# Optimization experiments

Measured on AMD Instinct MI355X. Metric: run time of the kernel, lower is better.

The kernel has to match this reference:

```python
import jax, jax.numpy as jnp
import numpy as np

D = 2048       # hidden / input / output width
DEPTH = 9      # infinite_depth (layer default)


def _infinite_layer(x, inf_w, cls_w, cls_b):
    """Faithful vectorized InfiniteNeuralLayer.forward.

    Original per-(sample, j, depth) Python loops build a circulant rotation
    matrix M = cos*I + sin*(shift_down - shift_up) and apply it 3x per depth
    with angles inf_w[depth, j, 0..2]. The rotated state never depends on x,
    so we carry one state row per output index j and scan over the 27 angle
    steps, expressing M @ s as cos*s + sin*(roll(s,1) - roll(s,-1)).
    infinite_biases is unused in the original forward and is omitted.
    """
    dim = x.shape[1]
    classical = x @ cls_w + cls_b                      # [B, dim]
    # angles per j per depth step: (DEPTH, dim_j, 3) -> sequence (DEPTH*3, dim_j)
    angles = jnp.transpose(inf_w[:, :, :3], (0, 2, 1)).reshape(-1, dim)
    init = jnp.full((dim, dim), 1.0 / np.sqrt(dim), dtype=x.dtype)  # [j, state]

    def step(s, a):
        c = jnp.cos(a)[:, None]
        sn = jnp.sin(a)[:, None]
        s_new = c * s + sn * (jnp.roll(s, 1, axis=1) - jnp.roll(s, -1, axis=1))
        return s_new, None

    state, _ = jax.lax.scan(step, init, angles)        # [dim_j, dim]
    p = state[:, 0] ** 2                               # |state[0]|^2 per j
    return jnp.tanh(classical + p[None, :])            # broadcast over batch


def setup_inputs() -> dict:
    key = jax.random.key(0)
    ks = jax.random.split(key, 16)
    s = 0.02  # keep activations in sane range (original uses raw randn)
    f = jax.random.normal
    return {
        "x":      f(ks[0], (2048, D), dtype=jnp.float32),
        "w0":     f(ks[1], (D, D), dtype=jnp.float32) * s,
        "b0":     f(ks[2], (D,), dtype=jnp.float32) * s,
        "w1":     f(ks[3], (D, D), dtype=jnp.float32) * s,
        "b1":     f(ks[4], (D,), dtype=jnp.float32) * s,
        "inf_w1": f(ks[5], (DEPTH, D, D), dtype=jnp.float32),
        "cls_w1": f(ks[6], (D, D), dtype=jnp.float32) * s,
        "cls_b1": f(ks[7], (D,), dtype=jnp.float32) * s,
        "w2":     f(ks[8], (D, D), dtype=jnp.float32) * s,
        "b2":     f(ks[9], (D,), dtype=jnp.float32) * s,
        "inf_w2": f(ks[10], (DEPTH, D, D), dtype=jnp.float32),
        "cls_w2": f(ks[11], (D, D), dtype=jnp.float32) * s,
        "cls_b2": f(ks[12], (D,), dtype=jnp.float32) * s,
        "w3":     f(ks[13], (D, D), dtype=jnp.float32) * s,
        "b3":     f(ks[14], (D,), dtype=jnp.float32) * s,
    }


def reference(x, w0, b0, w1, b1, inf_w1, cls_w1, cls_b1,
              w2, b2, inf_w2, cls_w2, cls_b2, w3, b3):
    h = jax.nn.relu(x @ w0 + b0)
    h = jax.nn.relu(h @ w1 + b1)
    h = _infinite_layer(h, inf_w1, cls_w1, cls_b1)
    h = jax.nn.relu(h @ w2 + b2)
    h = _infinite_layer(h, inf_w2, cls_w2, cls_b2)
    return jax.nn.relu(h @ w3 + b3)
```

## Files before the change

kernel.cpp:

```cpp
#include <hip/hip_runtime.h>
#include <hip/hip_bf16.h>


#define DD 2048
#define DEPTH 9

#define BM 128
#define BN 64
#define BK 64
#define NT (DD / BK)
#define ABUF (BM * BK)
#define BBUF (BN * BK)

typedef __attribute__((ext_vector_type(8))) short short8;
typedef __attribute__((ext_vector_type(4))) float f32x4;

__device__ __forceinline__ unsigned short f2bf(float f) {
  unsigned u = __float_as_uint(f);
  u += 0x7FFFu + ((u >> 16) & 1u);
  return (unsigned short)(u >> 16);
}

__global__ __launch_bounds__(256) void prep_kernel(
    const float* __restrict__ w0, const float* __restrict__ w1,
    unsigned short* __restrict__ wts, const float* __restrict__ x,
    unsigned short* __restrict__ xb, const float* __restrict__ infw1,
    const float* __restrict__ infw2, const float* __restrict__ clsb1,
    const float* __restrict__ clsb2, float* __restrict__ padd1,
    float* __restrict__ padd2) {
  int b = blockIdx.x;
  int tid = threadIdx.x;
  if (b < 8192) {
    __shared__ float tile[32][33];
    int z = b >> 12;
    int t = b & 4095;
    const float* src = z ? w1 : w0;
    unsigned short* dst = wts + (size_t)z * DD * DD;
    int bx = (t & 63) * 32;
    int by = (t >> 6) * 32;
    int tx = tid & 31, ty = tid >> 5;
#pragma unroll
    for (int i = ty; i < 32; i += 8)
      tile[i][tx] = src[(size_t)(by + i) * DD + bx + tx];
    __syncthreads();
#pragma unroll
    for (int i = ty; i < 32; i += 8)
      dst[(size_t)(bx + i) * DD + by + tx] = f2bf(tile[tx][i]);
  } else if (b < 12288) {
    int i = (b - 8192) * 256 + tid;
    float4 v = reinterpret_cast<const float4*>(x)[i];
    ushort4 o;
    o.x = f2bf(v.x); o.y = f2bf(v.y); o.z = f2bf(v.z); o.w = f2bf(v.w);
    reinterpret_cast<ushort4*>(xb)[i] = o;
  } else {
    int jj = (b - 12288) * 256 + tid;
    int layer = jj >> 11;
    int j = jj & 2047;
    const float* inf_w = layer ? infw2 : infw1;
    const float* cls_b = layer ? clsb2 : clsb1;
    float* padd = layer ? padd2 : padd1;
    float prod = 1.0f;
#pragma unroll
    for (int d = 0; d < DEPTH; ++d) {
      const float* row = inf_w + ((size_t)d * DD + j) * DD;
      prod *= cosf(row[0]) * cosf(row[1]) * cosf(row[2]);
    }
    padd[j] = cls_b[j] + prod * prod * (1.0f / (float)DD);
  }
}


__device__ __forceinline__ void gload_lds16(const unsigned short* g,
                                            unsigned short* l) {
  __builtin_amdgcn_global_load_lds(
      (const __attribute__((address_space(1))) void*)g,
      (__attribute__((address_space(3))) void*)l, 16, 0, 0);
}

template <int EPI>
__global__ __launch_bounds__(256) void gemm_kernel(
    const unsigned short* __restrict__ A, const unsigned short* __restrict__ Bt,
    const float* __restrict__ bias, unsigned short* __restrict__ Cb,
    float* __restrict__ Cf, const float* __restrict__ tsrc,
    unsigned short* __restrict__ tdst) {
  const int N = DD, K = DD;
  __shared__ __align__(16) unsigned char smem[73728];
  unsigned short* As = (unsigned short*)smem;
  unsigned short* Bs = (unsigned short*)(smem + 3 * ABUF * 2);

  int tid = threadIdx.x;
  int wid = tid >> 6, lane = tid & 63;
  int wr = wid >> 1, wc = wid & 1;
  int lr = lane & 15;
  int lg = lane >> 4;

  int bid = blockIdx.x;
  int swz = (bid & 7) * 64 + (bid >> 3);
  int bcol = (swz & 31) * BN;
  int brow = (swz >> 5) * BM;

  const unsigned short* Abase = A + (size_t)brow * K;
  const unsigned short* Bbase = Bt + (size_t)bcol * K;

  auto stage = [&](int buf, int tile) {
    int kt = tile * BK;
#pragma unroll
    for (int r = 0; r < 4; ++r) {
      int chunk = r * 256 + tid;
      int row = chunk >> 3;
      int sp = chunk & 7;
      int kof = (sp ^ ((row >> 1) & 7)) * 8;
      gload_lds16(Abase + (size_t)row * K + kt + kof,
                  As + buf * ABUF + (size_t)(r * 256 + wid * 64) * 8);
    }
#pragma unroll
    for (int r = 0; r < 2; ++r) {
      int chunk = r * 256 + tid;
      int row = chunk >> 3;
      int sp = chunk & 7;
      int kof = (sp ^ ((row >> 1) & 7)) * 8;
      gload_lds16(Bbase + (size_t)row * K + kt + kof,
                  Bs + buf * BBUF + (size_t)(r * 256 + wid * 64) * 8);
    }
  };

  f32x4 acc[4][2];
#pragma unroll
  for (int i = 0; i < 4; ++i)
#pragma unroll
    for (int j = 0; j < 2; ++j) acc[i][j] = f32x4{0.f, 0.f, 0.f, 0.f};

  auto compute = [&](int buf) {
#pragma unroll
    for (int ks = 0; ks < 2; ++ks) {
      short8 a[4], b[2];
#pragma unroll
      for (int mt = 0; mt < 4; ++mt) {
        int row = wr * 64 + mt * 16 + lr;
        int slot = (ks * 4 + lg) ^ ((row >> 1) & 7);
        a[mt] = *reinterpret_cast<const short8*>(
            &As[buf * ABUF + row * BK + slot * 8]);
      }
#pragma unroll
      for (int nt = 0; nt < 2; ++nt) {
        int row = wc * 32 + nt * 16 + lr;
        int slot = (ks * 4 + lg) ^ ((row >> 1) & 7);
        b[nt] = *reinterpret_cast<const short8*>(
            &Bs[buf * BBUF + row * BK + slot * 8]);
      }
      __builtin_amdgcn_s_setprio(1);
#pragma unroll
      for (int mt = 0; mt < 4; ++mt)
#pragma unroll
        for (int nt = 0; nt < 2; ++nt)
          acc[mt][nt] = __builtin_amdgcn_mfma_f32_16x16x32_bf16(
              a[mt], b[nt], acc[mt][nt], 0, 0, 0);
      __builtin_amdgcn_s_setprio(0);
    }
  };

  auto step = [&](int buf, int pf_tile, int wcase) {
    if (wcase == 0) asm volatile("s_waitcnt vmcnt(12)" ::: "memory");
    else if (wcase == 1) asm volatile("s_waitcnt vmcnt(6)" ::: "memory");
    else asm volatile("s_waitcnt vmcnt(0)" ::: "memory");
    __builtin_amdgcn_s_barrier();
    __builtin_amdgcn_sched_barrier(0);
    compute(buf);
    asm volatile("s_waitcnt lgkmcnt(0)" ::: "memory");
    __builtin_amdgcn_s_barrier();
    __builtin_amdgcn_sched_barrier(0);
    if (pf_tile < NT) stage(pf_tile % 3, pf_tile);
  };

  stage(0, 0); stage(1, 1); stage(2, 2);
#pragma unroll 1
  for (int i = 0; i < 10; ++i) {
    int t = 3 * i;
    step(0, t + 3, 0);
    step(1, t + 4, 0);
    step(2, t + 5, 0);
  }
  step(0, NT, 1);
  step(1, NT, 2);

  {
    float* et = reinterpret_cast<float*>(smem);
    __syncthreads();
#pragma unroll
    for (int nt = 0; nt < 2; ++nt) {
      int colb = wc * 32 + nt * 16 + lr;
      float bs = bias[bcol + colb];
#pragma unroll
      for (int mt = 0; mt < 4; ++mt) {
#pragma unroll
        for (int i = 0; i < 4; ++i) {
          int rowb = wr * 64 + mt * 16 + lg * 4 + i;
          float v = acc[mt][nt][i] + bs;
          v = (EPI == 1) ? tanhf(v) : fmaxf(v, 0.0f);
          et[rowb * 68 + colb] = v;
        }
      }
    }
    __syncthreads();
#pragma unroll
    for (int it = 0; it < 4; ++it) {
      int chunk = it * 256 + tid;
      int rowb = chunk >> 3;
      int c8 = (chunk & 7) * 8;
      float4 v0 = *reinterpret_cast<const float4*>(&et[rowb * 68 + c8]);
      float4 v1 = *reinterpret_cast<const float4*>(&et[rowb * 68 + c8 + 4]);
      size_t g = (size_t)(brow + rowb) * N + bcol + c8;
      if (EPI == 2) {
        *reinterpret_cast<float4*>(&Cf[g]) = v0;
        *reinterpret_cast<float4*>(&Cf[g + 4]) = v1;
      } else {
        uint4 o;
        o.x = (unsigned)f2bf(v0.x) | ((unsigned)f2bf(v0.y) << 16);
        o.y = (unsigned)f2bf(v0.z) | ((unsigned)f2bf(v0.w) << 16);
        o.z = (unsigned)f2bf(v1.x) | ((unsigned)f2bf(v1.y) << 16);
        o.w = (unsigned)f2bf(v1.z) | ((unsigned)f2bf(v1.w) << 16);
        *reinterpret_cast<uint4*>(&Cb[g]) = o;
      }
    }
  }

  if (tsrc != nullptr) {
    float* ft = reinterpret_cast<float*>(smem);
    __syncthreads();
#pragma unroll 1
    for (int t2 = 0; t2 < 2; ++t2) {
      int tau = bid * 2 + t2;
      int bx = (tau & 31) * 64;
      int by = (tau >> 5) * 64;
      if (t2) __syncthreads();
#pragma unroll
      for (int it = 0; it < 4; ++it) {
        int idx = it * 256 + tid;
        int r = idx >> 4, c4 = (idx & 15) * 4;
        float4 v = *reinterpret_cast<const float4*>(
            &tsrc[(size_t)(by + r) * DD + bx + c4]);
        ft[r * 65 + c4 + 0] = v.x;
        ft[r * 65 + c4 + 1] = v.y;
        ft[r * 65 + c4 + 2] = v.z;
        ft[r * 65 + c4 + 3] = v.w;
      }
      __syncthreads();
#pragma unroll
      for (int it = 0; it < 4; ++it) {
        int idx = it * 256 + tid;
        int n = idx >> 4, kq = idx & 15;
        ushort4 o;
        o.x = f2bf(ft[(kq * 4 + 0) * 65 + n]);
        o.y = f2bf(ft[(kq * 4 + 1) * 65 + n]);
        o.z = f2bf(ft[(kq * 4 + 2) * 65 + n]);
        o.w = f2bf(ft[(kq * 4 + 3) * 65 + n]);
        *reinterpret_cast<ushort4*>(&tdst[(size_t)(bx + n) * DD + by + kq * 4]) = o;
      }
    }
  }
}


extern "C" void kernel_launch(void* const* d_in, const int* in_sizes, int n_in,
                              void* d_out, int out_size, void* d_ws,
                              size_t ws_size, hipStream_t stream) {
  const float* x     = (const float*)d_in[0];
  const float* w0    = (const float*)d_in[1];
  const float* b0    = (const float*)d_in[2];
  const float* w1    = (const float*)d_in[3];
  const float* b1    = (const float*)d_in[4];
  const float* infw1 = (const float*)d_in[5];
  const float* clsw1 = (const float*)d_in[6];
  const float* clsb1 = (const float*)d_in[7];
  const float* w2    = (const float*)d_in[8];
  const float* b2    = (const float*)d_in[9];
  const float* infw2 = (const float*)d_in[10];
  const float* clsw2 = (const float*)d_in[11];
  const float* clsb2 = (const float*)d_in[12];
  const float* w3    = (const float*)d_in[13];
  const float* b3    = (const float*)d_in[14];
  float* out = (float*)d_out;

  char* ws = (char*)d_ws;
  const size_t MB = 1ull << 20;
  const size_t DDe = (size_t)DD * DD;
  unsigned short* buf0 = (unsigned short*)ws;
  unsigned short* buf1 = (unsigned short*)(ws + 8 * MB);
  unsigned short* wts  = (unsigned short*)(ws + 16 * MB);
  float* padd1 = (float*)(ws + 64 * MB);
  float* padd2 = padd1 + DD;

  prep_kernel<<<12304, 256, 0, stream>>>(w0, w1, wts, x, buf0, infw1, infw2,
                                         clsb1, clsb2, padd1, padd2);

  dim3 gg((DD / BM) * (DD / BN));
  gemm_kernel<0><<<gg, 256, 0, stream>>>(buf0, wts + 0 * DDe, b0,    buf1,
                                         nullptr, clsw1, wts + 2 * DDe);
  gemm_kernel<0><<<gg, 256, 0, stream>>>(buf1, wts + 1 * DDe, b1,    buf0,
                                         nullptr, w2,    wts + 3 * DDe);
  gemm_kernel<1><<<gg, 256, 0, stream>>>(buf0, wts + 2 * DDe, padd1, buf1,
                                         nullptr, clsw2, wts + 4 * DDe);
  gemm_kernel<0><<<gg, 256, 0, stream>>>(buf1, wts + 3 * DDe, b2,    buf0,
                                         nullptr, w3,    wts + 5 * DDe);
  gemm_kernel<1><<<gg, 256, 0, stream>>>(buf0, wts + 4 * DDe, padd2, buf1,
                                         nullptr, nullptr, nullptr);
  gemm_kernel<2><<<gg, 256, 0, stream>>>(buf1, wts + 5 * DDe, b3,    nullptr,
                                         out, nullptr, nullptr);
}
```

Measured before the change: 184.6 us.

## Enlarge GEMM tile to 128x128 with 8 waves splitting K

Widens the block tile from 128x64 to 128x128 and runs it with 512 threads. The 8 waves are arranged as four 64x64 output quadrants, each split across two waves that handle the two K halves of every 64-wide tile. Partial sums are reduced through LDS in the epilogue before bias and activation are applied. This raises operand reuse per loaded byte and halves the block count. In exchange it adds a cross-wave reduction, uses more LDS and more accumulator registers, and redistributes the transpose side-work over fewer blocks.

```diff
diff --git a/kernel.cpp b/kernel.cpp
--- a/kernel.cpp
+++ b/kernel.cpp
@@ -6,7 +6,7 @@
 #define DEPTH 9
 
 #define BM 128
-#define BN 64
+#define BN 128
 #define BK 64
 #define NT (DD / BK)
 #define ABUF (BM * BK)
@@ -78,26 +78,28 @@
 }
 
 template <int EPI>
-__global__ __launch_bounds__(256) void gemm_kernel(
+__global__ __launch_bounds__(512, 2) void gemm_kernel(
     const unsigned short* __restrict__ A, const unsigned short* __restrict__ Bt,
     const float* __restrict__ bias, unsigned short* __restrict__ Cb,
     float* __restrict__ Cf, const float* __restrict__ tsrc,
     unsigned short* __restrict__ tdst) {
   const int N = DD, K = DD;
-  __shared__ __align__(16) unsigned char smem[73728];
+  __shared__ __align__(16) unsigned char smem[98304];
   unsigned short* As = (unsigned short*)smem;
   unsigned short* Bs = (unsigned short*)(smem + 3 * ABUF * 2);
 
   int tid = threadIdx.x;
   int wid = tid >> 6, lane = tid & 63;
-  int wr = wid >> 1, wc = wid & 1;
+  int pos = wid >> 1;
+  int h = wid & 1;
+  int pr = pos >> 1, pc = pos & 1;
   int lr = lane & 15;
   int lg = lane >> 4;
 
   int bid = blockIdx.x;
-  int swz = (bid & 7) * 64 + (bid >> 3);
-  int bcol = (swz & 31) * BN;
-  int brow = (swz >> 5) * BM;
+  int swz = (bid & 7) * 32 + (bid >> 3);
+  int bcol = (swz & 15) * BN;
+  int brow = (swz >> 4) * BM;
 
   const unsigned short* Abase = A + (size_t)brow * K;
   const unsigned short* Bbase = Bt + (size_t)bcol * K;
@@ -105,63 +107,60 @@
   auto stage = [&](int buf, int tile) {
     int kt = tile * BK;
 #pragma unroll
-    for (int r = 0; r < 4; ++r) {
-      int chunk = r * 256 + tid;
+    for (int r = 0; r < 2; ++r) {
+      int chunk = r * 512 + tid;
       int row = chunk >> 3;
       int sp = chunk & 7;
       int kof = (sp ^ ((row >> 1) & 7)) * 8;
       gload_lds16(Abase + (size_t)row * K + kt + kof,
-                  As + buf * ABUF + (size_t)(r * 256 + wid * 64) * 8);
+                  As + buf * ABUF + (size_t)(r * 512 + wid * 64) * 8);
     }
 #pragma unroll
     for (int r = 0; r < 2; ++r) {
-      int chunk = r * 256 + tid;
+      int chunk = r * 512 + tid;
       int row = chunk >> 3;
       int sp = chunk & 7;
       int kof = (sp ^ ((row >> 1) & 7)) * 8;
       gload_lds16(Bbase + (size_t)row * K + kt + kof,
-                  Bs + buf * BBUF + (size_t)(r * 256 + wid * 64) * 8);
+                  Bs + buf * BBUF + (size_t)(r * 512 + wid * 64) * 8);
     }
   };
 
-  f32x4 acc[4][2];
+  f32x4 acc[4][4];
 #pragma unroll
   for (int i = 0; i < 4; ++i)
 #pragma unroll
-    for (int j = 0; j < 2; ++j) acc[i][j] = f32x4{0.f, 0.f, 0.f, 0.f};
+    for (int j = 0; j < 4; ++j) acc[i][j] = f32x4{0.f, 0.f, 0.f, 0.f};
 
   auto compute = [&](int buf) {
-#pragma unroll
-    for (int ks = 0; ks < 2; ++ks) {
-      short8 a[4], b[2];
-#pragma unroll
-      for (int mt = 0; mt < 4; ++mt) {
-        int row = wr * 64 + mt * 16 + lr;
-        int slot = (ks * 4 + lg) ^ ((row >> 1) & 7);
-        a[mt] = *reinterpret_cast<const short8*>(
-            &As[buf * ABUF + row * BK + slot * 8]);
-      }
-#pragma unroll
-      for (int nt = 0; nt < 2; ++nt) {
-        int row = wc * 32 + nt * 16 + lr;
-        int slot = (ks * 4 + lg) ^ ((row >> 1) & 7);
-        b[nt] = *reinterpret_cast<const short8*>(
-            &Bs[buf * BBUF + row * BK + slot * 8]);
-      }
-      __builtin_amdgcn_s_setprio(1);
-#pragma unroll
-      for (int mt = 0; mt < 4; ++mt)
-#pragma unroll
-        for (int nt = 0; nt < 2; ++nt)
-          acc[mt][nt] = __builtin_amdgcn_mfma_f32_16x16x32_bf16(
-              a[mt], b[nt], acc[mt][nt], 0, 0, 0);
-      __builtin_amdgcn_s_setprio(0);
-    }
+    short8 a[4], b[4];
+#pragma unroll
+    for (int mt = 0; mt < 4; ++mt) {
+      int row = pr * 64 + mt * 16 + lr;
+      int slot = (h * 4 + lg) ^ ((row >> 1) & 7);
+      a[mt] = *reinterpret_cast<const short8*>(
+          &As[buf * ABUF + row * BK + slot * 8]);
+    }
+#pragma unroll
+    for (int nt = 0; nt < 4; ++nt) {
+      int row = pc * 64 + nt * 16 + lr;
+      int slot = (h * 4 + lg) ^ ((row >> 1) & 7);
+      b[nt] = *reinterpret_cast<const short8*>(
+          &Bs[buf * BBUF + row * BK + slot * 8]);
+    }
+    __builtin_amdgcn_s_setprio(1);
+#pragma unroll
+    for (int mt = 0; mt < 4; ++mt)
+#pragma unroll
+      for (int nt = 0; nt < 4; ++nt)
+        acc[mt][nt] = __builtin_amdgcn_mfma_f32_16x16x32_bf16(
+            a[mt], b[nt], acc[mt][nt], 0, 0, 0);
+    __builtin_amdgcn_s_setprio(0);
   };
 
   auto step = [&](int buf, int pf_tile, int wcase) {
-    if (wcase == 0) asm volatile("s_waitcnt vmcnt(12)" ::: "memory");
-    else if (wcase == 1) asm volatile("s_waitcnt vmcnt(6)" ::: "memory");
+    if (wcase == 0) asm volatile("s_waitcnt vmcnt(8)" ::: "memory");
+    else if (wcase == 1) asm volatile("s_waitcnt vmcnt(4)" ::: "memory");
     else asm volatile("s_waitcnt vmcnt(0)" ::: "memory");
     __builtin_amdgcn_s_barrier();
     __builtin_amdgcn_sched_barrier(0);
@@ -186,29 +185,46 @@
   {
     float* et = reinterpret_cast<float*>(smem);
     __syncthreads();
-#pragma unroll
-    for (int nt = 0; nt < 2; ++nt) {
-      int colb = wc * 32 + nt * 16 + lr;
-      float bs = bias[bcol + colb];
-#pragma unroll
-      for (int mt = 0; mt < 4; ++mt) {
-#pragma unroll
-        for (int i = 0; i < 4; ++i) {
-          int rowb = wr * 64 + mt * 16 + lg * 4 + i;
-          float v = acc[mt][nt][i] + bs;
-          v = (EPI == 1) ? tanhf(v) : fmaxf(v, 0.0f);
-          et[rowb * 68 + colb] = v;
+    if (h == 0) {
+#pragma unroll
+      for (int nt = 0; nt < 4; ++nt) {
+        int colb = pc * 64 + nt * 16 + lr;
+#pragma unroll
+        for (int mt = 0; mt < 4; ++mt) {
+#pragma unroll
+          for (int i = 0; i < 4; ++i) {
+            int rowb = pr * 64 + mt * 16 + lg * 4 + i;
+            et[rowb * 132 + colb] = acc[mt][nt][i];
+          }
         }
       }
     }
     __syncthreads();
+    if (h == 1) {
+#pragma unroll
+      for (int nt = 0; nt < 4; ++nt) {
+        int colb = pc * 64 + nt * 16 + lr;
+        float bs = bias[bcol + colb];
+#pragma unroll
+        for (int mt = 0; mt < 4; ++mt) {
+#pragma unroll
+          for (int i = 0; i < 4; ++i) {
+            int rowb = pr * 64 + mt * 16 + lg * 4 + i;
+            float v = et[rowb * 132 + colb] + acc[mt][nt][i] + bs;
+            v = (EPI == 1) ? tanhf(v) : fmaxf(v, 0.0f);
+            et[rowb * 132 + colb] = v;
+          }
+        }
+      }
+    }
+    __syncthreads();
 #pragma unroll
     for (int it = 0; it < 4; ++it) {
-      int chunk = it * 256 + tid;
-      int rowb = chunk >> 3;
-      int c8 = (chunk & 7) * 8;
-      float4 v0 = *reinterpret_cast<const float4*>(&et[rowb * 68 + c8]);
-      float4 v1 = *reinterpret_cast<const float4*>(&et[rowb * 68 + c8 + 4]);
+      int chunk = it * 512 + tid;
+      int rowb = chunk >> 4;
+      int c8 = (chunk & 15) * 8;
+      float4 v0 = *reinterpret_cast<const float4*>(&et[rowb * 132 + c8]);
+      float4 v1 = *reinterpret_cast<const float4*>(&et[rowb * 132 + c8 + 4]);
       size_t g = (size_t)(brow + rowb) * N + bcol + c8;
       if (EPI == 2) {
         *reinterpret_cast<float4*>(&Cf[g]) = v0;
@@ -228,14 +244,14 @@
     float* ft = reinterpret_cast<float*>(smem);
     __syncthreads();
 #pragma unroll 1
-    for (int t2 = 0; t2 < 2; ++t2) {
-      int tau = bid * 2 + t2;
+    for (int t2 = 0; t2 < 4; ++t2) {
+      int tau = bid * 4 + t2;
       int bx = (tau & 31) * 64;
       int by = (tau >> 5) * 64;
       if (t2) __syncthreads();
 #pragma unroll
-      for (int it = 0; it < 4; ++it) {
-        int idx = it * 256 + tid;
+      for (int it = 0; it < 2; ++it) {
+        int idx = it * 512 + tid;
         int r = idx >> 4, c4 = (idx & 15) * 4;
         float4 v = *reinterpret_cast<const float4*>(
             &tsrc[(size_t)(by + r) * DD + bx + c4]);
@@ -246,8 +262,8 @@
       }
       __syncthreads();
 #pragma unroll
-      for (int it = 0; it < 4; ++it) {
-        int idx = it * 256 + tid;
+      for (int it = 0; it < 2; ++it) {
+        int idx = it * 512 + tid;
         int n = idx >> 4, kq = idx & 15;
         ushort4 o;
         o.x = f2bf(ft[(kq * 4 + 0) * 65 + n]);
@@ -294,16 +310,16 @@
                                          clsb1, clsb2, padd1, padd2);
 
   dim3 gg((DD / BM) * (DD / BN));
-  gemm_kernel<0><<<gg, 256, 0, stream>>>(buf0, wts + 0 * DDe, b0,    buf1,
+  gemm_kernel<0><<<gg, 512, 0, stream>>>(buf0, wts + 0 * DDe, b0,    buf1,
                                          nullptr, clsw1, wts + 2 * DDe);
-  gemm_kernel<0><<<gg, 256, 0, stream>>>(buf1, wts + 1 * DDe, b1,    buf0,
+  gemm_kernel<0><<<gg, 512, 0, stream>>>(buf1, wts + 1 * DDe, b1,    buf0,
                                          nullptr, w2,    wts + 3 * DDe);
-  gemm_kernel<1><<<gg, 256, 0, stream>>>(buf0, wts + 2 * DDe, padd1, buf1,
+  gemm_kernel<1><<<gg, 512, 0, stream>>>(buf0, wts + 2 * DDe, padd1, buf1,
                                          nullptr, clsw2, wts + 4 * DDe);
-  gemm_kernel<0><<<gg, 256, 0, stream>>>(buf1, wts + 3 * DDe, b2,    buf0,
+  gemm_kernel<0><<<gg, 512, 0, stream>>>(buf1, wts + 3 * DDe, b2,    buf0,
                                          nullptr, w3,    wts + 5 * DDe);
-  gemm_kernel<1><<<gg, 256, 0, stream>>>(buf0, wts + 4 * DDe, padd2, buf1,
+  gemm_kernel<1><<<gg, 512, 0, stream>>>(buf0, wts + 4 * DDe, padd2, buf1,
                                          nullptr, nullptr, nullptr);
-  gemm_kernel<2><<<gg, 256, 0, stream>>>(buf1, wts + 5 * DDe, b3,    nullptr,
+  gemm_kernel<2><<<gg, 512, 0, stream>>>(buf1, wts + 5 * DDe, b3,    nullptr,
                                          out, nullptr, nullptr);
 }
```

Result: slower. 192.2 us (+4.1%).
